# Kernel optimization log

Hardware: AMD Instinct MI355X
Metric: run time of the kernel (lower is better)

Reference implementation:

```python
import jax, jax.numpy as jnp
import numpy as np

RCUT, RCUT_SMTH = 6.0, 0.5
SEL = [32, 64]
SEC = [0, 32, 96]
PAIRS = [(0, 0), (0, 1), (1, 1)]  # (ti, tj) with ti <= tj, matching stacked weight index
NF, NLOC, NALL = 1, 256, 512
NNEI = sum(SEL)
NG = 96


def setup_inputs() -> dict:
    key = jax.random.key(0)
    ks = jax.random.split(key, 10)
    # coords in a 4A cube so most neighbor distances are inside rcut=6
    extended_coord = jax.random.uniform(ks[0], (NF, NALL * 3), dtype=jnp.float32) * 4.0
    nl = jax.random.randint(ks[1], (NF, NLOC, NNEI), 0, NALL - 1)
    # shift indices >= own local index by 1 to avoid self-neighbors (zero distance)
    nlist = nl + (nl >= jnp.arange(NLOC)[None, :, None]).astype(nl.dtype)
    extended_atype = jax.random.randint(ks[2], (NF, NALL), 0, 2)
    mean = jnp.zeros((2, NNEI, 4), jnp.float32)
    stddev = jnp.ones((2, NNEI, 4), jnp.float32)
    def w(k, shape, fan):
        return jax.random.normal(k, shape, jnp.float32) / np.float32(np.sqrt(fan))
    W1 = w(ks[3], (3, 1, 24), 1.0)
    b1 = 0.1 * jax.random.normal(ks[4], (3, 24), jnp.float32)
    W2 = w(ks[5], (3, 24, 48), 24.0)
    b2 = 0.1 * jax.random.normal(ks[6], (3, 48), jnp.float32)
    W3 = w(ks[7], (3, 48, 96), 48.0)
    b3 = 0.1 * jax.random.normal(ks[8], (3, 96), jnp.float32)
    return dict(nlist=nlist, extended_coord=extended_coord, extended_atype=extended_atype,
                mean=mean, stddev=stddev, W1=W1, b1=b1, W2=W2, b2=b2, W3=W3, b3=b3)


def _smooth_weight(r, rmin, rmax):
    uu = (r - rmin) / (rmax - rmin)
    vv = uu * uu * uu * (-6.0 * uu * uu + 15.0 * uu - 10.0) + 1.0
    return jnp.where(r <= rmin, 1.0, jnp.where(r >= rmax, 0.0, vv))


def _env_mat(nlist, coord, atype, mean, stddev):
    nf, nloc, nnei = nlist.shape
    coord = coord.reshape(nf, -1, 3)
    mask = nlist >= 0
    nl = jnp.where(mask, nlist, 0)
    # gather neighbor coords: nf x nloc x nnei x 3
    coord_r = jnp.take_along_axis(coord, nl.reshape(nf, -1, 1), axis=1).reshape(nf, nloc, nnei, 3)
    diff = coord_r - coord[:, :nloc, None, :]
    length = jnp.linalg.norm(diff, axis=-1, keepdims=True)
    length = length + (~mask)[..., None].astype(diff.dtype)  # avoid 0-div on padded entries
    t0 = 1.0 / length
    t1 = diff / (length * length)
    sw = _smooth_weight(length, RCUT_SMTH, RCUT) * mask[..., None].astype(diff.dtype)
    env = jnp.concatenate([t0, t1], axis=-1) * sw  # nf x nloc x nnei x 4
    loc_type = atype[:, :nloc]
    dmatrix = (env - mean[loc_type]) / stddev[loc_type]
    return dmatrix, sw


def _embed(x, W1, b1, W2, b2, W3, b3):
    # EmbeddingNet 1->24->48->96, tanh, resnet doubling residuals
    h1 = jnp.tanh(x @ W1 + b1)
    h2 = jnp.tanh(h1 @ W2 + b2) + jnp.concatenate([h1, h1], axis=-1)
    h3 = jnp.tanh(h2 @ W3 + b3) + jnp.concatenate([h2, h2], axis=-1)
    return h3


def reference(nlist, extended_coord, extended_atype, mean, stddev, W1, b1, W2, b2, W3, b3):
    nf, nloc, nnei = nlist.shape
    dmatrix, sw = _env_mat(nlist, extended_coord, extended_atype, mean, stddev)
    dm = dmatrix.reshape(nf * nloc, nnei, 4)
    result = jnp.zeros((nf * nloc, NG), dm.dtype)
    for p, (ti, tj) in enumerate(PAIRS):
        rr_i = dm[:, SEC[ti]:SEC[ti + 1], 1:]  # nfnl x nt_i x 3
        rr_j = dm[:, SEC[tj]:SEC[tj + 1], 1:]  # nfnl x nt_j x 3
        env_ij = jnp.einsum('ijm,ikm->ijk', rr_i, rr_j)  # nfnl x nt_i x nt_j
        gg = _embed(env_ij[..., None], W1[p], b1[p], W2[p], b2[p], W3[p], b3[p])
        res_ij = jnp.einsum('ijk,ijkm->im', env_ij, gg)
        result = result + res_ij * (1.0 / (SEL[ti] * SEL[tj]))
    return result.reshape(nf, nloc, NG)
```

## Files before the change

### kernel.cpp

```cpp
#include <hip/hip_runtime.h>

#define NLOC 256
#define NNEI 96
#define NG   96
#define S2LE 2.88539008177793f

typedef __attribute__((ext_vector_type(8))) short short8;
typedef __attribute__((ext_vector_type(4))) float f32x4;
union Frag { uint4 u; short8 s; };

__device__ __forceinline__ float tanh_sc(float s) {
    float e = __builtin_amdgcn_exp2f(s);
    return 1.0f - 2.0f * __builtin_amdgcn_rcpf(e + 1.0f);
}
__device__ __forceinline__ unsigned short f2bf(float f) {
    unsigned int u = __float_as_uint(f);
    u += 0x7FFFu + ((u >> 16) & 1u);
    return (unsigned short)(u >> 16);
}
__device__ __forceinline__ unsigned short f2bf_rhu(float f) {
    return (unsigned short)((__float_as_uint(f) + 0x8000u) >> 16);
}
__device__ __forceinline__ unsigned int pack_bf2(float lo, float hi) {
    unsigned int a = __float_as_uint(lo) + 0x8000u;
    unsigned int b = __float_as_uint(hi) + 0x8000u;
    return __builtin_amdgcn_perm(b, a, 0x07060302);
}
__device__ __forceinline__ void wave_fence() {
    asm volatile("s_waitcnt lgkmcnt(0)" ::: "memory");
    __builtin_amdgcn_sched_barrier(0);
}

__global__ __launch_bounds__(256) void prep_kernel(
        const float* __restrict__ W1, const float* __restrict__ b1,
        const float* __restrict__ W2, const float* __restrict__ b2,
        const float* __restrict__ W3, const float* __restrict__ b3,
        unsigned short* __restrict__ wf2, unsigned short* __restrict__ wf3,
        unsigned short* __restrict__ wfJ,
        float* __restrict__ w1s, float* __restrict__ b1s,
        float* __restrict__ b2s, float* __restrict__ b3s) {
    int t = blockIdx.x * blockDim.x + threadIdx.x;
    if (t < 2880) {
        int p = t / 960;
        int r = t % 960;
        int tile = r / 64;
        int l = r % 64;
        int nlo = l & 15, g = l >> 4;
        short8 v;
        if (tile < 3) {
            int nt = tile;
            #pragma unroll
            for (int j = 0; j < 8; j++) {
                int k = g * 8 + j;
                float w = (k < 24) ? W2[(p * 24 + k) * 48 + nt * 16 + nlo] * S2LE : 0.0f;
                v[j] = (short)f2bf(w);
            }
            *(short8*)(wf2 + ((p * 3 + nt) * 64 + l) * 8) = v;
        } else {
            int tt = tile - 3;
            int nt = tt >> 1, kc = tt & 1;
            #pragma unroll
            for (int j = 0; j < 8; j++) {
                int kk = (kc == 0) ? (g * 8 + j) : ((j < 4) ? (32 + g * 4 + j) : -1);
                float w = (kk >= 0) ? W3[(p * 48 + kk) * 96 + nt * 16 + nlo] * S2LE : 0.0f;
                v[j] = (short)f2bf(w);
            }
            *(short8*)(wf3 + ((p * 12 + nt * 2 + kc) * 64 + l) * 8) = v;
        }
    } else if (t < 3264) {
        int t2 = t - 2880;
        int f = t2 >> 6, l = t2 & 63;
        int ml = l & 15, g = l >> 4;
        short8 v;
        if (f < 3) {
            int c24 = (f * 16 + ml) % 24;
            #pragma unroll
            for (int j = 0; j < 8; j++)
                v[j] = (short)((g * 8 + j == c24) ? 0x3F80 : 0);
        } else {
            int nt2 = f - 3;
            if (nt2 < 2) {
                int c = nt2 * 16 + ml;
                #pragma unroll
                for (int j = 0; j < 8; j++)
                    v[j] = (short)((g * 8 + j == c) ? 0x3F80 : 0);
            } else {
                #pragma unroll
                for (int j = 0; j < 8; j++)
                    v[j] = (short)((j < 4 && (g * 4 + j) == ml) ? 0x3F80 : 0);
            }
        }
        *(short8*)(wfJ + (f * 64 + l) * 8) = v;
    } else if (t < 3768) {
        int u = t - 3264;
        if (u < 72)       { w1s[u] = W1[u] * S2LE; b1s[u] = b1[u] * S2LE; }
        else if (u < 216) { b2s[u - 72]  = b2[u - 72]  * S2LE; }
        else              { b3s[u - 216] = b3[u - 216] * S2LE; }
    }
}

__launch_bounds__(256, 4)
__global__ void mlp_kernel(const int* __restrict__ nlist, const float* __restrict__ coord,
                           const int* __restrict__ atype,
                           const float* __restrict__ mean, const float* __restrict__ stddev,
                           const float* __restrict__ w1s, const float* __restrict__ b1s,
                           const float* __restrict__ b2s, const float* __restrict__ b3s,
                           const unsigned short* __restrict__ wf2,
                           const unsigned short* __restrict__ wf3,
                           const unsigned short* __restrict__ wfJ,
                           float* __restrict__ out) {
    __shared__ __align__(16) unsigned char smem[40080];
    unsigned short* h1s = (unsigned short*)smem;
    unsigned short* h2s = (unsigned short*)(smem + 12304);
    float* rrl = (float*)(smem + 38928);
    unsigned char* h2b = (unsigned char*)h2s;

    int tid = threadIdx.x;
    int blk = blockIdx.x;
    int i = blk / 20;
    int b = blk - i * 20;

    int p, base_e, offi, offj, count, Aint;
    float scale;
    bool tri;
    if (b < 3)       { p=0; base_e=b*256;      offi=0;  offj=0;  scale=1.0f/1024.0f; count=528;  tri=true;  Aint=65;  }
    else if (b < 11) { p=1; base_e=(b-3)*256;  offi=0;  offj=32; scale=1.0f/2048.0f; count=2048; tri=false; Aint=0;   }
    else             { p=2; base_e=(b-11)*256; offi=32; offj=32; scale=1.0f/4096.0f; count=2080; tri=true;  Aint=129; }

    {
        uint4 z = make_uint4(0u, 0u, 0u, 0u);
        *(uint4*)(smem + tid * 48 +  0) = z;
        *(uint4*)(smem + tid * 48 + 16) = z;
        *(uint4*)(smem + tid * 48 + 32) = z;
        if (tid == 0) *(uint4*)(smem + 12288) = z;
        if (tid < NG) *(float*)(h2b + tid * 104 + 100) = 0.0f;
    }
    if (tid < NNEI) {
        int n = tid;
        int idx = nlist[i * NNEI + n];
        bool msk = idx >= 0;
        int safe = msk ? idx : 0;
        float cx = coord[i*3], cy = coord[i*3+1], cz = coord[i*3+2];
        float dx = coord[safe*3]   - cx;
        float dy = coord[safe*3+1] - cy;
        float dz = coord[safe*3+2] - cz;
        float rn = sqrtf(dx*dx + dy*dy + dz*dz) + (msk ? 0.0f : 1.0f);
        float sw;
        if (rn <= 0.5f)      sw = 1.0f;
        else if (rn >= 6.0f) sw = 0.0f;
        else {
            float uu = (rn - 0.5f) * (1.0f / 5.5f);
            sw = uu*uu*uu*(uu*(-6.0f*uu + 15.0f) - 10.0f) + 1.0f;
        }
        if (!msk) sw = 0.0f;
        float ir2 = 1.0f / (rn * rn);
        int ty = atype[i];
        const float* mu = mean   + (ty * NNEI + n) * 4;
        const float* sd = stddev + (ty * NNEI + n) * 4;
        rrl[n*3+0] = (dx * ir2 * sw - mu[1]) / sd[1];
        rrl[n*3+1] = (dy * ir2 * sw - mu[2]) / sd[2];
        rrl[n*3+2] = (dz * ir2 * sw - mu[3]) / sd[3];
    }
    __syncthreads();

    float xs;
    {
        int e = base_e + tid;
        bool valid = e < count;
        int ec = valid ? e : 0;
        int jj, kk;
        float mult = 1.0f;
        if (!tri) { jj = ec >> 6; kk = ec & 63; }
        else {
            float Af = (float)Aint;
            int j = (int)((Af - sqrtf(Af*Af - 8.0f*(float)ec)) * 0.5f);
            int Tj1 = ((j+1)*(Aint-j-1)) >> 1;
            if (ec >= Tj1) j++;
            int Tj = (j*(Aint-j)) >> 1;
            if (ec < Tj) { j--; Tj = (j*(Aint-j)) >> 1; }
            jj = j; kk = j + (ec - Tj);
            mult = (jj == kk) ? 1.0f : 2.0f;
        }
        const float* ri = rrl + (offi + jj) * 3;
        const float* rj = rrl + (offj + kk) * 3;
        float x = ri[0]*rj[0] + ri[1]*rj[1] + ri[2]*rj[2];
        x = valid ? x : 0.0f;
        xs = x * mult;

        const float* w1 = w1s + p * 24;
        const float* c1 = b1s + p * 24;
        float h1v[24];
        #pragma unroll
        for (int u = 0; u < 24; u++)
            h1v[u] = tanh_sc(fmaf(x, w1[u], c1[u]));
        #pragma unroll
        for (int t8 = 0; t8 < 3; t8++) {
            uint4 q = make_uint4(pack_bf2(h1v[8*t8+0], h1v[8*t8+1]),
                                 pack_bf2(h1v[8*t8+2], h1v[8*t8+3]),
                                 pack_bf2(h1v[8*t8+4], h1v[8*t8+5]),
                                 pack_bf2(h1v[8*t8+6], h1v[8*t8+7]));
            *(uint4*)(h1s + tid*24 + 8*t8) = q;
        }
    }
    *(float*)(h2b + tid*104 + 96) = xs;
    wave_fence();

    int l  = tid & 63;
    int w  = tid >> 6;
    int ml = l & 15, g = l >> 4;

    short8 bw2[3], jf2[3];
    float  b2c[3];
    #pragma unroll
    for (int nt = 0; nt < 3; nt++) {
        bw2[nt] = *(const short8*)(wf2 + ((p*3 + nt)*64 + l)*8);
        jf2[nt] = *(const short8*)(wfJ + (nt*64 + l)*8);
        b2c[nt] = b2s[p*48 + nt*16 + ml];
    }
    #pragma unroll
    for (int mi = 0; mi < 4; mi++) {
        int mt = w*4 + mi;
        int arow = mt*16 + ml;
        uint2 lo = *(const uint2*)(h1s + arow*24 + g*8);
        uint2 hi = *(const uint2*)(h1s + arow*24 + g*8 + 4);
        Frag fa; fa.u = make_uint4(lo.x, lo.y, hi.x, hi.y);
        #pragma unroll
        for (int nt = 0; nt < 3; nt++) {
            f32x4 bini = {b2c[nt], b2c[nt], b2c[nt], b2c[nt]};
            f32x4 zz   = {0.f, 0.f, 0.f, 0.f};
            f32x4 acc = __builtin_amdgcn_mfma_f32_16x16x32_bf16(fa.s, bw2[nt], bini, 0, 0, 0);
            f32x4 aj  = __builtin_amdgcn_mfma_f32_16x16x32_bf16(fa.s, jf2[nt], zz,   0, 0, 0);
            int col = nt*16 + ml;
            #pragma unroll
            for (int r = 0; r < 4; r++) {
                int orow = mt*16 + g*4 + r;
                float v = tanh_sc(acc[r]) + aj[r];
                h2s[orow*52 + col] = f2bf_rhu(v);
            }
        }
    }
    wave_fence();

    short8 a3a[4], a3b[4];
    float  xv[4][4];
    #pragma unroll
    for (int mi = 0; mi < 4; mi++) {
        int mt = w*4 + mi;
        int arow = mt*16 + ml;
        uint2 lo = *(const uint2*)(h2s + arow*52 + g*8);
        uint2 hi = *(const uint2*)(h2s + arow*52 + g*8 + 4);
        Frag fa; fa.u = make_uint4(lo.x, lo.y, hi.x, hi.y);
        a3a[mi] = fa.s;
        uint2 t2 = *(const uint2*)(h2s + arow*52 + 32 + g*4);
        Frag fb; fb.u = make_uint4(t2.x, t2.y, 0u, 0u);
        a3b[mi] = fb.s;
        #pragma unroll
        for (int r = 0; r < 4; r++)
            xv[mi][r] = *(const float*)(h2b + (mt*16 + g*4 + r)*104 + 96);
    }
    short8 jf3[3];
    #pragma unroll
    for (int q = 0; q < 3; q++)
        jf3[q] = *(const short8*)(wfJ + ((3 + q)*64 + l)*8);

    #pragma unroll
    for (int nt2 = 0; nt2 < 3; nt2++) {
        f32x4 zz = {0.f, 0.f, 0.f, 0.f};
        f32x4 ajp[4];
        #pragma unroll
        for (int mi = 0; mi < 4; mi++) {
            f32x4 a = __builtin_amdgcn_mfma_f32_16x16x32_bf16(
                (nt2 == 2) ? a3b[mi] : a3a[mi], jf3[nt2], zz, 0, 0, 0);
            ajp[mi] = a + 1.0f;
        }
        #pragma unroll
        for (int h = 0; h < 2; h++) {
            int nt = nt2 + 3*h;
            short8 b30 = *(const short8*)(wf3 + ((p*12 + nt*2 + 0)*64 + l)*8);
            short8 b31 = *(const short8*)(wf3 + ((p*12 + nt*2 + 1)*64 + l)*8);
            float b3c = b3s[p*96 + nt*16 + ml];
            float facc = 0.0f;
            #pragma unroll
            for (int mi = 0; mi < 4; mi++) {
                f32x4 bini = {b3c, b3c, b3c, b3c};
                f32x4 acc = __builtin_amdgcn_mfma_f32_16x16x32_bf16(a3a[mi], b30, bini, 0, 0, 0);
                acc = __builtin_amdgcn_mfma_f32_16x16x32_bf16(a3b[mi], b31, acc, 0, 0, 0);
                #pragma unroll
                for (int r = 0; r < 4; r++) {
                    float e2 = __builtin_amdgcn_exp2f(acc[r]);
                    float rc = __builtin_amdgcn_rcpf(e2 + 1.0f);
                    float h3 = fmaf(-2.0f, rc, ajp[mi][r]);
                    facc = fmaf(xv[mi][r], h3, facc);
                }
            }
            facc += __shfl_xor(facc, 16, 64);
            facc += __shfl_xor(facc, 32, 64);
            if (g == 0) atomicAdd((float*)(h2b + (nt*16 + ml)*104 + 100), facc);
        }
    }
    __syncthreads();
    if (tid < NG)
        atomicAdd(&out[i*NG + tid], *(const float*)(h2b + tid*104 + 100) * scale);
}

extern "C" void kernel_launch(void* const* d_in, const int* in_sizes, int n_in,
                              void* d_out, int out_size, void* d_ws, size_t ws_size,
                              hipStream_t stream) {
    const int*   nlist  = (const int*)  d_in[0];
    const float* coord  = (const float*)d_in[1];
    const int*   atype  = (const int*)  d_in[2];
    const float* mean   = (const float*)d_in[3];
    const float* stddev = (const float*)d_in[4];
    const float* W1     = (const float*)d_in[5];
    const float* b1     = (const float*)d_in[6];
    const float* W2     = (const float*)d_in[7];
    const float* b2     = (const float*)d_in[8];
    const float* W3     = (const float*)d_in[9];
    const float* b3     = (const float*)d_in[10];
    float* out = (float*)d_out;

    char* ws = (char*)d_ws;
    unsigned short* wf2 = (unsigned short*)(ws + 0);
    unsigned short* wf3 = (unsigned short*)(ws + 9216);
    unsigned short* wfJ = (unsigned short*)(ws + 46080);
    float* w1s = (float*)(ws + 52224);
    float* b1s = (float*)(ws + 52512);
    float* b2s = (float*)(ws + 52800);
    float* b3s = (float*)(ws + 53376);

    prep_kernel<<<15, 256, 0, stream>>>(W1, b1, W2, b2, W3, b3,
                                        wf2, wf3, wfJ, w1s, b1s, b2s, b3s);
    mlp_kernel<<<NLOC * 20, 256, 0, stream>>>(
        nlist, coord, atype, mean, stddev,
        w1s, b1s, b2s, b3s, wf2, wf3, wfJ, out);
}
```

Measured before the change: 138.7 us.

## Build layer-1 fragments in registers via bpermute, shrink LDS for higher occupancy

Removes the h1 shared-memory staging buffer. Layer-1 activations are now computed directly in MFMA A-fragment order using shuffles and ds_bpermute, and the environment vectors and x values are packed into spare slots of the h2 buffer. This cuts LDS from about 40KB to 26KB and raises the launch-bounds occupancy target from 4 to 6 blocks. The per-block LDS reduction and final __syncthreads are replaced by direct per-wave global atomics on the output. Bias-plus-one is folded into the MFMA accumulator init. The trade-off is more global atomics and register pressure under the tighter launch bound.

```diff
diff --git a/kernel.cpp b/kernel.cpp
--- a/kernel.cpp
+++ b/kernel.cpp
@@ -99,7 +99,7 @@
     }
 }
 
-__launch_bounds__(256, 4)
+__launch_bounds__(256, 6)
 __global__ void mlp_kernel(const int* __restrict__ nlist, const float* __restrict__ coord,
                            const int* __restrict__ atype,
                            const float* __restrict__ mean, const float* __restrict__ stddev,
@@ -109,11 +109,9 @@
                            const unsigned short* __restrict__ wf3,
                            const unsigned short* __restrict__ wfJ,
                            float* __restrict__ out) {
-    __shared__ __align__(16) unsigned char smem[40080];
-    unsigned short* h1s = (unsigned short*)smem;
-    unsigned short* h2s = (unsigned short*)(smem + 12304);
-    float* rrl = (float*)(smem + 38928);
-    unsigned char* h2b = (unsigned char*)h2s;
+    __shared__ __align__(16) unsigned char smem[26624];
+    unsigned short* h2s = (unsigned short*)smem;
+    unsigned char*  h2b = smem;
 
     int tid = threadIdx.x;
     int blk = blockIdx.x;
@@ -127,14 +125,10 @@
     else if (b < 11) { p=1; base_e=(b-3)*256;  offi=0;  offj=32; scale=1.0f/2048.0f; count=2048; tri=false; Aint=0;   }
     else             { p=2; base_e=(b-11)*256; offi=32; offj=32; scale=1.0f/4096.0f; count=2080; tri=true;  Aint=129; }
 
-    {
-        uint4 z = make_uint4(0u, 0u, 0u, 0u);
-        *(uint4*)(smem + tid * 48 +  0) = z;
-        *(uint4*)(smem + tid * 48 + 16) = z;
-        *(uint4*)(smem + tid * 48 + 32) = z;
-        if (tid == 0) *(uint4*)(smem + 12288) = z;
-        if (tid < NG) *(float*)(h2b + tid * 104 + 100) = 0.0f;
-    }
+    int l  = tid & 63;
+    int w  = tid >> 6;
+    int ml = l & 15, g = l >> 4;
+
     if (tid < NNEI) {
         int n = tid;
         int idx = nlist[i * NNEI + n];
@@ -157,13 +151,16 @@
         int ty = atype[i];
         const float* mu = mean   + (ty * NNEI + n) * 4;
         const float* sd = stddev + (ty * NNEI + n) * 4;
-        rrl[n*3+0] = (dx * ir2 * sw - mu[1]) / sd[1];
-        rrl[n*3+1] = (dy * ir2 * sw - mu[2]) / sd[2];
-        rrl[n*3+2] = (dz * ir2 * sw - mu[3]) / sd[3];
+        float vx = (dx * ir2 * sw - mu[1]) / sd[1];
+        float vy = (dy * ir2 * sw - mu[2]) / sd[2];
+        float vz = (dz * ir2 * sw - mu[3]) / sd[3];
+        float* hp = (float*)(h2b + (96 + n) * 104 + 96);
+        hp[0] = vx; hp[1] = vy;
+        *(float*)(h2b + (192 + (n >> 1)) * 104 + 96 + ((n & 1) << 2)) = vz;
     }
     __syncthreads();
 
-    float xs;
+    float xs, xown;
     {
         int e = base_e + tid;
         bool valid = e < count;
@@ -181,33 +178,44 @@
             jj = j; kk = j + (ec - Tj);
             mult = (jj == kk) ? 1.0f : 2.0f;
         }
-        const float* ri = rrl + (offi + jj) * 3;
-        const float* rj = rrl + (offj + kk) * 3;
-        float x = ri[0]*rj[0] + ri[1]*rj[1] + ri[2]*rj[2];
+        int ja = offi + jj, kb = offj + kk;
+        const float* pa = (const float*)(h2b + (96 + ja) * 104 + 96);
+        const float* pb = (const float*)(h2b + (96 + kb) * 104 + 96);
+        float az = *(const float*)(h2b + (192 + (ja >> 1)) * 104 + 96 + ((ja & 1) << 2));
+        float bz = *(const float*)(h2b + (192 + (kb >> 1)) * 104 + 96 + ((kb & 1) << 2));
+        float x = pa[0]*pb[0] + pa[1]*pb[1] + az*bz;
         x = valid ? x : 0.0f;
-        xs = x * mult;
-
-        const float* w1 = w1s + p * 24;
-        const float* c1 = b1s + p * 24;
-        float h1v[24];
-        #pragma unroll
-        for (int u = 0; u < 24; u++)
-            h1v[u] = tanh_sc(fmaf(x, w1[u], c1[u]));
-        #pragma unroll
-        for (int t8 = 0; t8 < 3; t8++) {
-            uint4 q = make_uint4(pack_bf2(h1v[8*t8+0], h1v[8*t8+1]),
-                                 pack_bf2(h1v[8*t8+2], h1v[8*t8+3]),
-                                 pack_bf2(h1v[8*t8+4], h1v[8*t8+5]),
-                                 pack_bf2(h1v[8*t8+6], h1v[8*t8+7]));
-            *(uint4*)(h1s + tid*24 + 8*t8) = q;
-        }
-    }
-    *(float*)(h2b + tid*104 + 96) = xs;
-    wave_fence();
-
-    int l  = tid & 63;
-    int w  = tid >> 6;
-    int ml = l & 15, g = l >> 4;
+        xown = x;
+        xs = x * mult * scale;
+    }
+    unsigned int Wx[3][4];
+    #pragma unroll
+    for (int s = 0; s < 3; s++) {
+        int idx = s * 64 + l;
+        int mi4 = (idx * 1366) >> 16;
+        int rem = idx - mi4 * 48;
+        int gg  = rem >> 4;
+        int r64 = mi4 * 16 + (rem & 15);
+        float xr = __shfl(xown, r64, 64);
+        const float* wp = w1s + p * 24 + gg * 8;
+        const float* bp = b1s + p * 24 + gg * 8;
+        float4 wa = *(const float4*)wp;
+        float4 wb = *(const float4*)(wp + 4);
+        float4 ba = *(const float4*)bp;
+        float4 bb = *(const float4*)(bp + 4);
+        float h0 = tanh_sc(fmaf(xr, wa.x, ba.x));
+        float h1 = tanh_sc(fmaf(xr, wa.y, ba.y));
+        float h2 = tanh_sc(fmaf(xr, wa.z, ba.z));
+        float h3 = tanh_sc(fmaf(xr, wa.w, ba.w));
+        float h4 = tanh_sc(fmaf(xr, wb.x, bb.x));
+        float h5 = tanh_sc(fmaf(xr, wb.y, bb.y));
+        float h6 = tanh_sc(fmaf(xr, wb.z, bb.z));
+        float h7 = tanh_sc(fmaf(xr, wb.w, bb.w));
+        Wx[s][0] = pack_bf2(h0, h1);
+        Wx[s][1] = pack_bf2(h2, h3);
+        Wx[s][2] = pack_bf2(h4, h5);
+        Wx[s][3] = pack_bf2(h6, h7);
+    }
 
     short8 bw2[3], jf2[3];
     float  b2c[3];
@@ -217,24 +225,44 @@
         jf2[nt] = *(const short8*)(wfJ + (nt*64 + l)*8);
         b2c[nt] = b2s[p*48 + nt*16 + ml];
     }
+    int  bsel = l - ((l >= 48) ? 16 : 0);
+    bool cg0  = (g == 0);
+    bool cg01 = (g <= 1);
+    f32x4 ones = {1.f, 1.f, 1.f, 1.f};
     #pragma unroll
     for (int mi = 0; mi < 4; mi++) {
-        int mt = w*4 + mi;
-        int arow = mt*16 + ml;
-        uint2 lo = *(const uint2*)(h1s + arow*24 + g*8);
-        uint2 hi = *(const uint2*)(h1s + arow*24 + g*8 + 4);
-        Frag fa; fa.u = make_uint4(lo.x, lo.y, hi.x, hi.y);
+        int a4 = ((mi * 48 + bsel) & 63) << 2;
+        unsigned int fw[4];
+        #pragma unroll
+        for (int j = 0; j < 4; j++) {
+            if (mi == 0) {
+                fw[j] = (unsigned)__builtin_amdgcn_ds_bpermute(a4, (int)Wx[0][j]);
+            } else if (mi == 3) {
+                fw[j] = (unsigned)__builtin_amdgcn_ds_bpermute(a4, (int)Wx[2][j]);
+            } else if (mi == 1) {
+                unsigned v0 = (unsigned)__builtin_amdgcn_ds_bpermute(a4, (int)Wx[0][j]);
+                unsigned v1 = (unsigned)__builtin_amdgcn_ds_bpermute(a4, (int)Wx[1][j]);
+                fw[j] = cg0 ? v0 : v1;
+            } else {
+                unsigned v0 = (unsigned)__builtin_amdgcn_ds_bpermute(a4, (int)Wx[1][j]);
+                unsigned v1 = (unsigned)__builtin_amdgcn_ds_bpermute(a4, (int)Wx[2][j]);
+                fw[j] = cg01 ? v0 : v1;
+            }
+        }
+        Frag fa; fa.u = make_uint4(fw[0], fw[1], fw[2], fw[3]);
+        int mt = w * 4 + mi;
         #pragma unroll
         for (int nt = 0; nt < 3; nt++) {
             f32x4 bini = {b2c[nt], b2c[nt], b2c[nt], b2c[nt]};
-            f32x4 zz   = {0.f, 0.f, 0.f, 0.f};
             f32x4 acc = __builtin_amdgcn_mfma_f32_16x16x32_bf16(fa.s, bw2[nt], bini, 0, 0, 0);
-            f32x4 aj  = __builtin_amdgcn_mfma_f32_16x16x32_bf16(fa.s, jf2[nt], zz,   0, 0, 0);
+            f32x4 aj  = __builtin_amdgcn_mfma_f32_16x16x32_bf16(fa.s, jf2[nt], ones, 0, 0, 0);
             int col = nt*16 + ml;
             #pragma unroll
             for (int r = 0; r < 4; r++) {
                 int orow = mt*16 + g*4 + r;
-                float v = tanh_sc(acc[r]) + aj[r];
+                float e2 = __builtin_amdgcn_exp2f(acc[r]);
+                float rc = __builtin_amdgcn_rcpf(e2 + 1.0f);
+                float v  = fmaf(-2.0f, rc, aj[r]);
                 h2s[orow*52 + col] = f2bf_rhu(v);
             }
         }
@@ -254,9 +282,11 @@
         uint2 t2 = *(const uint2*)(h2s + arow*52 + 32 + g*4);
         Frag fb; fb.u = make_uint4(t2.x, t2.y, 0u, 0u);
         a3b[mi] = fb.s;
+        int xb = (l & 48) + mi * 64;
         #pragma unroll
         for (int r = 0; r < 4; r++)
-            xv[mi][r] = *(const float*)(h2b + (mt*16 + g*4 + r)*104 + 96);
+            xv[mi][r] = __int_as_float(
+                __builtin_amdgcn_ds_bpermute(xb + r*4, __float_as_int(xs)));
     }
     short8 jf3[3];
     #pragma unroll
@@ -265,14 +295,11 @@
 
     #pragma unroll
     for (int nt2 = 0; nt2 < 3; nt2++) {
-        f32x4 zz = {0.f, 0.f, 0.f, 0.f};
         f32x4 ajp[4];
         #pragma unroll
-        for (int mi = 0; mi < 4; mi++) {
-            f32x4 a = __builtin_amdgcn_mfma_f32_16x16x32_bf16(
-                (nt2 == 2) ? a3b[mi] : a3a[mi], jf3[nt2], zz, 0, 0, 0);
-            ajp[mi] = a + 1.0f;
-        }
+        for (int mi = 0; mi < 4; mi++)
+            ajp[mi] = __builtin_amdgcn_mfma_f32_16x16x32_bf16(
+                (nt2 == 2) ? a3b[mi] : a3a[mi], jf3[nt2], ones, 0, 0, 0);
         #pragma unroll
         for (int h = 0; h < 2; h++) {
             int nt = nt2 + 3*h;
@@ -295,12 +322,9 @@
             }
             facc += __shfl_xor(facc, 16, 64);
             facc += __shfl_xor(facc, 32, 64);
-            if (g == 0) atomicAdd((float*)(h2b + (nt*16 + ml)*104 + 100), facc);
-        }
-    }
-    __syncthreads();
-    if (tid < NG)
-        atomicAdd(&out[i*NG + tid], *(const float*)(h2b + tid*104 + 100) * scale);
+            if (l < 16) atomicAdd(&out[i*NG + nt*16 + ml], facc);
+        }
+    }
 }
 
 extern "C" void kernel_launch(void* const* d_in, const int* in_sizes, int n_in,
```

Result: slower. 188.2 us (+35.7%).

## Precompute env vectors in prep kernel, drop smem zeroing and LDS atomics

Applied to the files above, without the earlier changes.

Each atom's normalized neighbor vectors are now computed once in extra prep blocks and written to a float4 workspace buffer. Previously each of the 20 blocks per atom recomputed them in shared memory before a barrier. The mlp kernel no longer zeroes shared memory. The residual +1 is folded into the MFMA accumulator init, and the scale is applied to x up front. x is passed through ds_bpermute instead of an LDS round-trip, and per-wave partials go to shared memory without LDS atomics before the final reduction. When the workspace is too small, a fallback template keeps the in-kernel path. Dropping the min-waves launch bound may change register allocation and occupancy.

```diff
diff --git a/kernel.cpp b/kernel.cpp
--- a/kernel.cpp
+++ b/kernel.cpp
@@ -38,105 +38,15 @@
         unsigned short* __restrict__ wf2, unsigned short* __restrict__ wf3,
         unsigned short* __restrict__ wfJ,
         float* __restrict__ w1s, float* __restrict__ b1s,
-        float* __restrict__ b2s, float* __restrict__ b3s) {
-    int t = blockIdx.x * blockDim.x + threadIdx.x;
-    if (t < 2880) {
-        int p = t / 960;
-        int r = t % 960;
-        int tile = r / 64;
-        int l = r % 64;
-        int nlo = l & 15, g = l >> 4;
-        short8 v;
-        if (tile < 3) {
-            int nt = tile;
-            #pragma unroll
-            for (int j = 0; j < 8; j++) {
-                int k = g * 8 + j;
-                float w = (k < 24) ? W2[(p * 24 + k) * 48 + nt * 16 + nlo] * S2LE : 0.0f;
-                v[j] = (short)f2bf(w);
-            }
-            *(short8*)(wf2 + ((p * 3 + nt) * 64 + l) * 8) = v;
-        } else {
-            int tt = tile - 3;
-            int nt = tt >> 1, kc = tt & 1;
-            #pragma unroll
-            for (int j = 0; j < 8; j++) {
-                int kk = (kc == 0) ? (g * 8 + j) : ((j < 4) ? (32 + g * 4 + j) : -1);
-                float w = (kk >= 0) ? W3[(p * 48 + kk) * 96 + nt * 16 + nlo] * S2LE : 0.0f;
-                v[j] = (short)f2bf(w);
-            }
-            *(short8*)(wf3 + ((p * 12 + nt * 2 + kc) * 64 + l) * 8) = v;
-        }
-    } else if (t < 3264) {
-        int t2 = t - 2880;
-        int f = t2 >> 6, l = t2 & 63;
-        int ml = l & 15, g = l >> 4;
-        short8 v;
-        if (f < 3) {
-            int c24 = (f * 16 + ml) % 24;
-            #pragma unroll
-            for (int j = 0; j < 8; j++)
-                v[j] = (short)((g * 8 + j == c24) ? 0x3F80 : 0);
-        } else {
-            int nt2 = f - 3;
-            if (nt2 < 2) {
-                int c = nt2 * 16 + ml;
-                #pragma unroll
-                for (int j = 0; j < 8; j++)
-                    v[j] = (short)((g * 8 + j == c) ? 0x3F80 : 0);
-            } else {
-                #pragma unroll
-                for (int j = 0; j < 8; j++)
-                    v[j] = (short)((j < 4 && (g * 4 + j) == ml) ? 0x3F80 : 0);
-            }
-        }
-        *(short8*)(wfJ + (f * 64 + l) * 8) = v;
-    } else if (t < 3768) {
-        int u = t - 3264;
-        if (u < 72)       { w1s[u] = W1[u] * S2LE; b1s[u] = b1[u] * S2LE; }
-        else if (u < 216) { b2s[u - 72]  = b2[u - 72]  * S2LE; }
-        else              { b3s[u - 216] = b3[u - 216] * S2LE; }
-    }
-}
-
-__launch_bounds__(256, 4)
-__global__ void mlp_kernel(const int* __restrict__ nlist, const float* __restrict__ coord,
-                           const int* __restrict__ atype,
-                           const float* __restrict__ mean, const float* __restrict__ stddev,
-                           const float* __restrict__ w1s, const float* __restrict__ b1s,
-                           const float* __restrict__ b2s, const float* __restrict__ b3s,
-                           const unsigned short* __restrict__ wf2,
-                           const unsigned short* __restrict__ wf3,
-                           const unsigned short* __restrict__ wfJ,
-                           float* __restrict__ out) {
-    __shared__ __align__(16) unsigned char smem[40080];
-    unsigned short* h1s = (unsigned short*)smem;
-    unsigned short* h2s = (unsigned short*)(smem + 12304);
-    float* rrl = (float*)(smem + 38928);
-    unsigned char* h2b = (unsigned char*)h2s;
-
-    int tid = threadIdx.x;
-    int blk = blockIdx.x;
-    int i = blk / 20;
-    int b = blk - i * 20;
-
-    int p, base_e, offi, offj, count, Aint;
-    float scale;
-    bool tri;
-    if (b < 3)       { p=0; base_e=b*256;      offi=0;  offj=0;  scale=1.0f/1024.0f; count=528;  tri=true;  Aint=65;  }
-    else if (b < 11) { p=1; base_e=(b-3)*256;  offi=0;  offj=32; scale=1.0f/2048.0f; count=2048; tri=false; Aint=0;   }
-    else             { p=2; base_e=(b-11)*256; offi=32; offj=32; scale=1.0f/4096.0f; count=2080; tri=true;  Aint=129; }
-
-    {
-        uint4 z = make_uint4(0u, 0u, 0u, 0u);
-        *(uint4*)(smem + tid * 48 +  0) = z;
-        *(uint4*)(smem + tid * 48 + 16) = z;
-        *(uint4*)(smem + tid * 48 + 32) = z;
-        if (tid == 0) *(uint4*)(smem + 12288) = z;
-        if (tid < NG) *(float*)(h2b + tid * 104 + 100) = 0.0f;
-    }
-    if (tid < NNEI) {
-        int n = tid;
+        float* __restrict__ b2s, float* __restrict__ b3s,
+        const int* __restrict__ nlist, const float* __restrict__ coord,
+        const int* __restrict__ atype,
+        const float* __restrict__ mean, const float* __restrict__ stddev,
+        float4* __restrict__ rrle) {
+    if (blockIdx.x >= 15) {
+        if (rrle == nullptr) return;
+        int t = (blockIdx.x - 15) * 256 + threadIdx.x;
+        int i = t / 96, n = t - i * 96;
         int idx = nlist[i * NNEI + n];
         bool msk = idx >= 0;
         int safe = msk ? idx : 0;
@@ -157,11 +67,138 @@
         int ty = atype[i];
         const float* mu = mean   + (ty * NNEI + n) * 4;
         const float* sd = stddev + (ty * NNEI + n) * 4;
-        rrl[n*3+0] = (dx * ir2 * sw - mu[1]) / sd[1];
-        rrl[n*3+1] = (dy * ir2 * sw - mu[2]) / sd[2];
-        rrl[n*3+2] = (dz * ir2 * sw - mu[3]) / sd[3];
-    }
-    __syncthreads();
+        float vx = (dx * ir2 * sw - mu[1]) / sd[1];
+        float vy = (dy * ir2 * sw - mu[2]) / sd[2];
+        float vz = (dz * ir2 * sw - mu[3]) / sd[3];
+        rrle[t] = make_float4(vx, vy, vz, 0.0f);
+        return;
+    }
+    int t = blockIdx.x * blockDim.x + threadIdx.x;
+    if (t < 2880) {
+        int p = t / 960;
+        int r = t % 960;
+        int tile = r / 64;
+        int l = r % 64;
+        int nlo = l & 15, g = l >> 4;
+        short8 v;
+        if (tile < 3) {
+            int nt = tile;
+            #pragma unroll
+            for (int j = 0; j < 8; j++) {
+                int k = g * 8 + j;
+                float w = (k < 24) ? W2[(p * 24 + k) * 48 + nt * 16 + nlo] * S2LE : 0.0f;
+                v[j] = (short)f2bf(w);
+            }
+            *(short8*)(wf2 + ((p * 3 + nt) * 64 + l) * 8) = v;
+        } else {
+            int tt = tile - 3;
+            int nt = tt >> 1, kc = tt & 1;
+            #pragma unroll
+            for (int j = 0; j < 8; j++) {
+                int kk = (kc == 0) ? (g * 8 + j) : ((j < 4) ? (32 + g * 4 + j) : -1);
+                float w = (kk >= 0) ? W3[(p * 48 + kk) * 96 + nt * 16 + nlo] * S2LE : 0.0f;
+                v[j] = (short)f2bf(w);
+            }
+            *(short8*)(wf3 + ((p * 12 + nt * 2 + kc) * 64 + l) * 8) = v;
+        }
+    } else if (t < 3264) {
+        int t2 = t - 2880;
+        int f = t2 >> 6, l = t2 & 63;
+        int ml = l & 15, g = l >> 4;
+        short8 v;
+        if (f < 3) {
+            int c24 = (f * 16 + ml) % 24;
+            #pragma unroll
+            for (int j = 0; j < 8; j++)
+                v[j] = (short)((g * 8 + j == c24) ? 0x3F80 : 0);
+        } else {
+            int nt2 = f - 3;
+            if (nt2 < 2) {
+                int c = nt2 * 16 + ml;
+                #pragma unroll
+                for (int j = 0; j < 8; j++)
+                    v[j] = (short)((g * 8 + j == c) ? 0x3F80 : 0);
+            } else {
+                #pragma unroll
+                for (int j = 0; j < 8; j++)
+                    v[j] = (short)((j < 4 && (g * 4 + j) == ml) ? 0x3F80 : 0);
+            }
+        }
+        *(short8*)(wfJ + (f * 64 + l) * 8) = v;
+    } else if (t < 3768) {
+        int u = t - 3264;
+        if (u < 72)       { w1s[u] = W1[u] * S2LE; b1s[u] = b1[u] * S2LE; }
+        else if (u < 216) { b2s[u - 72]  = b2[u - 72]  * S2LE; }
+        else              { b3s[u - 216] = b3[u - 216] * S2LE; }
+    }
+}
+
+template<bool GR>
+__launch_bounds__(256)
+__global__ void mlp_kernel(const int* __restrict__ nlist, const float* __restrict__ coord,
+                           const int* __restrict__ atype,
+                           const float* __restrict__ mean, const float* __restrict__ stddev,
+                           const float* __restrict__ w1s, const float* __restrict__ b1s,
+                           const float* __restrict__ b2s, const float* __restrict__ b3s,
+                           const unsigned short* __restrict__ wf2,
+                           const unsigned short* __restrict__ wf3,
+                           const unsigned short* __restrict__ wfJ,
+                           const float4* __restrict__ rrle,
+                           float* __restrict__ out) {
+    __shared__ __align__(16) unsigned char smem[40448];
+    unsigned short* h1s = (unsigned short*)smem;
+    unsigned short* h2s = (unsigned short*)(smem + 12288);
+    float*          resf = (float*)(smem + 38912);
+    unsigned char*  h2b = smem + 12288;
+
+    int tid = threadIdx.x;
+    int blk = blockIdx.x;
+    int i = blk / 20;
+    int b = blk - i * 20;
+
+    int p, base_e, offi, offj, count, Aint;
+    float scale;
+    bool tri;
+    if (b < 3)       { p=0; base_e=b*256;      offi=0;  offj=0;  scale=1.0f/1024.0f; count=528;  tri=true;  Aint=65;  }
+    else if (b < 11) { p=1; base_e=(b-3)*256;  offi=0;  offj=32; scale=1.0f/2048.0f; count=2048; tri=false; Aint=0;   }
+    else             { p=2; base_e=(b-11)*256; offi=32; offj=32; scale=1.0f/4096.0f; count=2080; tri=true;  Aint=129; }
+
+    int l  = tid & 63;
+    int w  = tid >> 6;
+    int ml = l & 15, g = l >> 4;
+
+    if (!GR) {
+        if (tid < NNEI) {
+            int n = tid;
+            int idx = nlist[i * NNEI + n];
+            bool msk = idx >= 0;
+            int safe = msk ? idx : 0;
+            float cx = coord[i*3], cy = coord[i*3+1], cz = coord[i*3+2];
+            float dx = coord[safe*3]   - cx;
+            float dy = coord[safe*3+1] - cy;
+            float dz = coord[safe*3+2] - cz;
+            float rn = sqrtf(dx*dx + dy*dy + dz*dz) + (msk ? 0.0f : 1.0f);
+            float sw;
+            if (rn <= 0.5f)      sw = 1.0f;
+            else if (rn >= 6.0f) sw = 0.0f;
+            else {
+                float uu = (rn - 0.5f) * (1.0f / 5.5f);
+                sw = uu*uu*uu*(uu*(-6.0f*uu + 15.0f) - 10.0f) + 1.0f;
+            }
+            if (!msk) sw = 0.0f;
+            float ir2 = 1.0f / (rn * rn);
+            int ty = atype[i];
+            const float* mu = mean   + (ty * NNEI + n) * 4;
+            const float* sd = stddev + (ty * NNEI + n) * 4;
+            float vx = (dx * ir2 * sw - mu[1]) / sd[1];
+            float vy = (dy * ir2 * sw - mu[2]) / sd[2];
+            float vz = (dz * ir2 * sw - mu[3]) / sd[3];
+            float* hp = (float*)(h2b + (96 + n) * 104 + 96);
+            hp[0] = vx; hp[1] = vy;
+            *(float*)(h2b + (192 + (n >> 1)) * 104 + 96 + ((n & 1) << 2)) = vz;
+        }
+        __syncthreads();
+    }
 
     float xs;
     {
@@ -181,11 +218,21 @@
             jj = j; kk = j + (ec - Tj);
             mult = (jj == kk) ? 1.0f : 2.0f;
         }
-        const float* ri = rrl + (offi + jj) * 3;
-        const float* rj = rrl + (offj + kk) * 3;
-        float x = ri[0]*rj[0] + ri[1]*rj[1] + ri[2]*rj[2];
+        int ja = offi + jj, kb = offj + kk;
+        float x;
+        if (GR) {
+            float4 ra = rrle[i * NNEI + ja];
+            float4 rb = rrle[i * NNEI + kb];
+            x = ra.x*rb.x + ra.y*rb.y + ra.z*rb.z;
+        } else {
+            const float* pa = (const float*)(h2b + (96 + ja) * 104 + 96);
+            const float* pb = (const float*)(h2b + (96 + kb) * 104 + 96);
+            float az = *(const float*)(h2b + (192 + (ja >> 1)) * 104 + 96 + ((ja & 1) << 2));
+            float bz = *(const float*)(h2b + (192 + (kb >> 1)) * 104 + 96 + ((kb & 1) << 2));
+            x = pa[0]*pb[0] + pa[1]*pb[1] + az*bz;
+        }
         x = valid ? x : 0.0f;
-        xs = x * mult;
+        xs = x * mult * scale;
 
         const float* w1 = w1s + p * 24;
         const float* c1 = b1s + p * 24;
@@ -202,12 +249,7 @@
             *(uint4*)(h1s + tid*24 + 8*t8) = q;
         }
     }
-    *(float*)(h2b + tid*104 + 96) = xs;
     wave_fence();
-
-    int l  = tid & 63;
-    int w  = tid >> 6;
-    int ml = l & 15, g = l >> 4;
 
     short8 bw2[3], jf2[3];
     float  b2c[3];
@@ -217,24 +259,27 @@
         jf2[nt] = *(const short8*)(wfJ + (nt*64 + l)*8);
         b2c[nt] = b2s[p*48 + nt*16 + ml];
     }
+    f32x4 ones = {1.f, 1.f, 1.f, 1.f};
+    int aoff = (g == 3) ? 0 : g * 8;
     #pragma unroll
     for (int mi = 0; mi < 4; mi++) {
         int mt = w*4 + mi;
         int arow = mt*16 + ml;
-        uint2 lo = *(const uint2*)(h1s + arow*24 + g*8);
-        uint2 hi = *(const uint2*)(h1s + arow*24 + g*8 + 4);
+        uint2 lo = *(const uint2*)(h1s + arow*24 + aoff);
+        uint2 hi = *(const uint2*)(h1s + arow*24 + aoff + 4);
         Frag fa; fa.u = make_uint4(lo.x, lo.y, hi.x, hi.y);
         #pragma unroll
         for (int nt = 0; nt < 3; nt++) {
             f32x4 bini = {b2c[nt], b2c[nt], b2c[nt], b2c[nt]};
-            f32x4 zz   = {0.f, 0.f, 0.f, 0.f};
             f32x4 acc = __builtin_amdgcn_mfma_f32_16x16x32_bf16(fa.s, bw2[nt], bini, 0, 0, 0);
-            f32x4 aj  = __builtin_amdgcn_mfma_f32_16x16x32_bf16(fa.s, jf2[nt], zz,   0, 0, 0);
+            f32x4 aj  = __builtin_amdgcn_mfma_f32_16x16x32_bf16(fa.s, jf2[nt], ones, 0, 0, 0);
             int col = nt*16 + ml;
             #pragma unroll
             for (int r = 0; r < 4; r++) {
                 int orow = mt*16 + g*4 + r;
-                float v = tanh_sc(acc[r]) + aj[r];
+                float e2 = __builtin_amdgcn_exp2f(acc[r]);
+                float rc = __builtin_amdgcn_rcpf(e2 + 1.0f);
+                float v  = fmaf(-2.0f, rc, aj[r]);
                 h2s[orow*52 + col] = f2bf_rhu(v);
             }
         }
@@ -254,9 +299,11 @@
         uint2 t2 = *(const uint2*)(h2s + arow*52 + 32 + g*4);
         Frag fb; fb.u = make_uint4(t2.x, t2.y, 0u, 0u);
         a3b[mi] = fb.s;
+        int xb = (l & 48) + mi * 64;
         #pragma unroll
         for (int r = 0; r < 4; r++)
-            xv[mi][r] = *(const float*)(h2b + (mt*16 + g*4 + r)*104 + 96);
+            xv[mi][r] = __int_as_float(
+                __builtin_amdgcn_ds_bpermute(xb + r*4, __float_as_int(xs)));
     }
     short8 jf3[3];
     #pragma unroll
@@ -265,14 +312,11 @@
 
     #pragma unroll
     for (int nt2 = 0; nt2 < 3; nt2++) {
-        f32x4 zz = {0.f, 0.f, 0.f, 0.f};
         f32x4 ajp[4];
         #pragma unroll
-        for (int mi = 0; mi < 4; mi++) {
-            f32x4 a = __builtin_amdgcn_mfma_f32_16x16x32_bf16(
-                (nt2 == 2) ? a3b[mi] : a3a[mi], jf3[nt2], zz, 0, 0, 0);
-            ajp[mi] = a + 1.0f;
-        }
+        for (int mi = 0; mi < 4; mi++)
+            ajp[mi] = __builtin_amdgcn_mfma_f32_16x16x32_bf16(
+                (nt2 == 2) ? a3b[mi] : a3a[mi], jf3[nt2], ones, 0, 0, 0);
         #pragma unroll
         for (int h = 0; h < 2; h++) {
             int nt = nt2 + 3*h;
@@ -295,12 +339,14 @@
             }
             facc += __shfl_xor(facc, 16, 64);
             facc += __shfl_xor(facc, 32, 64);
-            if (g == 0) atomicAdd((float*)(h2b + (nt*16 + ml)*104 + 100), facc);
+            if (l < 16) resf[w*96 + nt*16 + ml] = facc;
         }
     }
     __syncthreads();
-    if (tid < NG)
-        atomicAdd(&out[i*NG + tid], *(const float*)(h2b + tid*104 + 100) * scale);
+    if (tid < NG) {
+        float s = resf[tid] + resf[96 + tid] + resf[192 + tid] + resf[288 + tid];
+        atomicAdd(&out[i*NG + tid], s);
+    }
 }
 
 extern "C" void kernel_launch(void* const* d_in, const int* in_sizes, int n_in,
@@ -327,10 +373,19 @@
     float* b1s = (float*)(ws + 52512);
     float* b2s = (float*)(ws + 52800);
     float* b3s = (float*)(ws + 53376);
-
-    prep_kernel<<<15, 256, 0, stream>>>(W1, b1, W2, b2, W3, b3,
-                                        wf2, wf3, wfJ, w1s, b1s, b2s, b3s);
-    mlp_kernel<<<NLOC * 20, 256, 0, stream>>>(
-        nlist, coord, atype, mean, stddev,
-        w1s, b1s, b2s, b3s, wf2, wf3, wfJ, out);
-}
+    size_t need = 55296 + (size_t)NLOC * NNEI * 16;
+    bool gr = ws_size >= need;
+    float4* rrle = gr ? (float4*)(ws + 55296) : nullptr;
+
+    prep_kernel<<<gr ? 111 : 15, 256, 0, stream>>>(
+        W1, b1, W2, b2, W3, b3, wf2, wf3, wfJ, w1s, b1s, b2s, b3s,
+        nlist, coord, atype, mean, stddev, rrle);
+    if (gr)
+        mlp_kernel<true><<<NLOC * 20, 256, 0, stream>>>(
+            nlist, coord, atype, mean, stddev,
+            w1s, b1s, b2s, b3s, wf2, wf3, wfJ, rrle, out);
+    else
+        mlp_kernel<false><<<NLOC * 20, 256, 0, stream>>>(
+            nlist, coord, atype, mean, stddev,
+            w1s, b1s, b2s, b3s, wf2, wf3, wfJ, rrle, out);
+}
```

New measurement: 135.2 us (median of 2 runs). 1.03x faster.
